# Kernel optimization log

Hardware: AMD Instinct MI355X
Metric: run time of the kernel (lower is better)

Reference implementation:

```python
import jax, jax.numpy as jnp
import numpy as np
from jax import lax

GRID = 200      # _FIXED_GRID_LEN
SOFT_K = 50.0   # _SOFT_MASK_K
BN_EPS = 1e-5


def setup_inputs() -> dict:
    key = jax.random.key(0)
    ks = jax.random.split(key, 12)
    B, L = 8192, 2001
    f32 = jnp.float32
    inp = {
        'phase': jax.random.uniform(ks[0], (B, L), f32, -1.0, 1.0),
        'primary_flux': 0.01 * jax.random.normal(ks[1], (B, L), f32),
        'secondary_flux': 0.01 * jax.random.normal(ks[2], (B, L), f32),
        'odd_even_diff': 0.01 * jax.random.normal(ks[3], (B, L), f32),
        # TaylorGateLayerV8 params
        'A': jnp.asarray(0.01, f32),
        'Bp': jnp.asarray(1.0, f32),
        't0': jnp.asarray(0.0, f32),
        # BatchNorm1d(4), eval mode (running stats)
        'bn_gamma': jnp.ones((4,), f32),
        'bn_beta': jnp.zeros((4,), f32),
        'bn_mean': jnp.zeros((4,), f32),
        'bn_var': jnp.ones((4,), f32),
        # Conv1d(4,8,7) / Conv1d(8,16,5)
        'conv1_w': 0.1 * jax.random.normal(ks[4], (8, 4, 7), f32),
        'conv1_b': jnp.zeros((8,), f32),
        'conv2_w': 0.1 * jax.random.normal(ks[5], (16, 8, 5), f32),
        'conv2_b': jnp.zeros((16,), f32),
        # Linear(21, 1)
        'fc_w': 0.1 * jax.random.normal(ks[6], (1, 21), f32),
        'fc_b': jnp.zeros((1,), f32),
    }
    return inp


def _conv1d(x, w, b, pad):
    # x: (B, C, L), w: (O, C, K)
    y = lax.conv_general_dilated(x, w, window_strides=(1,), padding=[(pad, pad)],
                                 dimension_numbers=('NCH', 'OIH', 'NCH'))
    return y + b[None, :, None]


def _interp_linear_ac(x, out_len):
    # torch F.interpolate(mode='linear', align_corners=True) on (B, L) -> (B, out_len)
    L = x.shape[1]
    pos = jnp.linspace(0.0, L - 1.0, out_len)
    i0 = jnp.floor(pos).astype(jnp.int32)
    i1 = jnp.minimum(i0 + 1, L - 1)
    w = (pos - i0).astype(x.dtype)
    return x[:, i0] * (1.0 - w) + x[:, i1] * w


def reference(phase, primary_flux, secondary_flux, odd_even_diff,
              A, Bp, t0, bn_gamma, bn_beta, bn_mean, bn_var,
              conv1_w, conv1_b, conv2_w, conv2_b, fc_w, fc_b):
    # --- TaylorGateLayerV8: 2nd-order Taylor U-shape transit template ---
    gate = -A * jnp.clip(1.0 - Bp * (phase - t0) ** 2, 0.0, None)

    # --- CNN branch ---
    x = jnp.stack([gate, primary_flux, secondary_flux, odd_even_diff], axis=1)  # (B,4,L)
    inv = bn_gamma / jnp.sqrt(bn_var + BN_EPS)
    x = x * inv[None, :, None] + (bn_beta - bn_mean * inv)[None, :, None]
    x = jax.nn.relu(_conv1d(x, conv1_w, conv1_b, 3))
    x = jax.nn.relu(_conv1d(x, conv2_w, conv2_b, 2))
    cnn_out = jnp.mean(x, axis=2)  # AdaptiveAvgPool1d(1) -> (B,16)

    # --- shape features ---
    batch = primary_flux.shape[0]
    A_abs = jnp.abs(A) + 1e-8
    depth = jnp.clip(-primary_flux, 0.0, None)
    depth_norm = depth / A_abs
    depth_rs = _interp_linear_ac(depth, GRID)  # (B, 200)
    dx = 2.0 / (GRID - 1)                       # trapz over linspace(-1,1,200)
    auc_raw = dx * (jnp.sum(depth_rs, axis=1) - 0.5 * (depth_rs[:, 0] + depth_rs[:, -1]))
    auc_norm = auc_raw / A_abs
    dip_all = jax.nn.sigmoid(SOFT_K * (depth_norm - 0.1))
    flat_bot = jax.nn.sigmoid(SOFT_K * (depth_norm - 0.8))
    ingress = dip_all - flat_bot
    total = 1.0 - dip_all + ingress + flat_bot + 1e-8
    ingress = ingress / total
    flat_bot = flat_bot / total
    t14 = jnp.mean(ingress + flat_bot, axis=1) + 1e-8
    t12_t14 = jnp.mean(ingress, axis=1) / t14
    flat_bottom = jnp.mean(flat_bot, axis=1)
    B_bcast = jnp.broadcast_to(Bp, (batch,)).astype(depth.dtype)
    shape = jnp.stack([B_bcast, auc_raw, auc_norm, t12_t14, flat_bottom], axis=1)  # (B,5)

    features = jnp.concatenate([cnn_out, shape], axis=1)  # (B,21)
    logits = features @ fc_w.T + fc_b
    return jax.nn.sigmoid(logits)
```

## Files before the change

### kernel.cpp

```cpp
#include <hip/hip_runtime.h>
#include <math.h>

#define L_LEN 2001
#define CCH 224
#define NCH 9
#define XRECS 256
#define YRECS 240
#define NTC 14

typedef __attribute__((ext_vector_type(8))) short bf16x8;
typedef __attribute__((ext_vector_type(4))) float f32x4;
typedef __attribute__((ext_vector_type(16))) float f32x16;
typedef __attribute__((ext_vector_type(4), aligned(4))) float f32x4u;
#if __has_builtin(__builtin_amdgcn_cvt_pk_bf16_f32)
typedef __attribute__((ext_vector_type(2))) __bf16 bf16x2_t;
#endif

union FragU { unsigned u[4]; uint2 u2[2]; uint4 u4; bf16x8 v; };

__device__ __forceinline__ unsigned short f2bf(float f) {
    unsigned u = __builtin_bit_cast(unsigned, f);
    u += 0x7fffu + ((u >> 16) & 1u);
    return (unsigned short)(u >> 16);
}
__device__ __forceinline__ unsigned bfpack(float lo, float hi) {
#if __has_builtin(__builtin_amdgcn_cvt_pk_bf16_f32)
    bf16x2_t r = __builtin_amdgcn_cvt_pk_bf16_f32(lo, hi);
    return __builtin_bit_cast(unsigned, r);
#else
    unsigned ul = __builtin_bit_cast(unsigned, lo);
    unsigned uh = __builtin_bit_cast(unsigned, hi);
    ul += 0x7fffu + ((ul >> 16) & 1u);
    uh += 0x7fffu + ((uh >> 16) & 1u);
    return __builtin_amdgcn_perm(uh, ul, 0x07060302);
#endif
}
__device__ __forceinline__ float fast_rcp(float x) { return __builtin_amdgcn_rcpf(x); }
__device__ __forceinline__ float fexp2(float x) {
#if __has_builtin(__builtin_amdgcn_exp2f)
    return __builtin_amdgcn_exp2f(x);
#else
    return __expf(x * 0.69314718f);
#endif
}

__global__ __launch_bounds__(256, 3)
void taylor_cnn_v11_wave(const float* __restrict__ phase, const float* __restrict__ primary,
                         const float* __restrict__ secondary, const float* __restrict__ oddeven,
                         const float* __restrict__ pA, const float* __restrict__ pBp,
                         const float* __restrict__ pT0,
                         const float* __restrict__ bng, const float* __restrict__ bnb,
                         const float* __restrict__ bnm, const float* __restrict__ bnv,
                         const float* __restrict__ w1, const float* __restrict__ b1,
                         const float* __restrict__ w2, const float* __restrict__ b2,
                         const float* __restrict__ fcw, const float* __restrict__ fcb,
                         float* __restrict__ out, int nrows)
{
    __shared__ __align__(16) unsigned int xs_i[4][XRECS * 2];
    __shared__ __align__(16) unsigned int y1_i[4][YRECS * 4];

    const int tid = threadIdx.x;
    const int l   = tid & 63;
    const int wid = tid >> 6;
    const int row = blockIdx.x * 4 + wid;
    if (row >= nrows) return;
    const long base = (long)row * L_LEN;

    unsigned int* xs = xs_i[wid];
    unsigned int* y1 = y1_i[wid];

    const int n    = l & 15;
    const int quad = l >> 4;
    const int c    = l & 31;
    const int h    = l >> 5;

    const float A  = pA[0];
    const float Bp = pBp[0];
    const float t0 = pT0[0];
    const float A_abs = fabsf(A) + 1e-8f;
    const float rAabs = 1.0f / A_abs;
    const float nBp  = -Bp;
    const float cExp = -72.134766f * rAabs;

    float inv1, inv2, inv3, gInv0, off0, off1, off2, off3;
    {
        float iv0 = bng[0] / sqrtf(bnv[0] + 1e-5f);
        float iv1 = bng[1] / sqrtf(bnv[1] + 1e-5f);
        float iv2 = bng[2] / sqrtf(bnv[2] + 1e-5f);
        float iv3 = bng[3] / sqrtf(bnv[3] + 1e-5f);
        gInv0 = -A * iv0;
        inv1 = iv1; inv2 = iv2; inv3 = iv3;
        off0 = bnb[0] - bnm[0] * iv0;
        off1 = bnb[1] - bnm[1] * iv1;
        off2 = bnb[2] - bnm[2] * iv2;
        off3 = bnb[3] - bnm[3] * iv3;
    }

    bf16x8 a32_0, a32_1;
#pragma unroll
    for (int jp = 0; jp < 8; ++jp) {
        int ch_  = jp & 3;
        int tap0 = (jp >> 2) + 2 * h;
        int tap1 = 4 + (jp >> 2) + 2 * h;
        float v0 = (c < 8) ? w1[(c * 4 + ch_) * 7 + tap0] : 0.0f;
        float v1 = (c < 8 && tap1 < 7) ? w1[(c * 4 + ch_) * 7 + tap1] : 0.0f;
        a32_0[jp] = (short)f2bf(v0);
        a32_1[jp] = (short)f2bf(v1);
    }
    f32x16 cb32;
#pragma unroll
    for (int r = 0; r < 16; ++r)
        cb32[r] = (r < 4) ? b1[(r & 3) + 4 * h] : 0.0f;

    bf16x8 a1;
#pragma unroll
    for (int jp = 0; jp < 8; ++jp) {
        int j = quad + 4 * (jp >> 2);
        int cc = jp & 3;
        float v = (n < 8 && j < 7) ? w1[(n * 4 + cc) * 7 + j] : 0.0f;
        a1[jp] = (short)f2bf(v);
    }
    bf16x8 a20, a21;
#pragma unroll
    for (int jp = 0; jp < 8; ++jp) {
        float v0 = w2[(n * 8 + jp) * 5 + quad];
        float v1 = (quad + 4 < 5) ? w2[(n * 8 + jp) * 5 + quad + 4] : 0.0f;
        a20[jp] = (short)f2bf(v0);
        a21[jp] = (short)f2bf(v1);
    }
    f32x4 cb1, cb2;
#pragma unroll
    for (int r = 0; r < 4; ++r) {
        cb1[r] = b1[(quad * 4 + r) & 7];
        cb2[r] = b2[quad * 4 + r];
    }
    float fw0 = fcw[quad * 4 + 0];
    float fw1 = fcw[quad * 4 + 1];
    float fw2 = fcw[quad * 4 + 2];
    float fw3 = fcw[quad * 4 + 3];

    float s_dip = 0.0f, s_fb = 0.0f;
    float m0 = 0.f, m1 = 0.f, m2 = 0.f, m3 = 0.f;

    float s_auc = 0.0f;
#pragma unroll
    for (int k = 0; k < 4; ++k) {
        int s = l + 64 * k;
        if (k < 3 || l < 8) {
            float pos = (float)s * (2000.0f / 199.0f);
            int i0 = (int)pos;
            if (i0 > 2000) i0 = 2000;
            int i1 = (i0 + 1 < L_LEN) ? i0 + 1 : 2000;
            float w  = pos - (float)i0;
            float d0 = fmaxf(-primary[base + i0], 0.f);
            float d1 = fmaxf(-primary[base + i1], 0.f);
            float v  = d0 * (1.0f - w) + d1 * w;
            float wt = (s == 0 || s == 199) ? 0.5f : 1.0f;
            s_auc += v * wt;
        }
    }

    auto aRec = [&](int m, int p, bool valid, bool core) {
        float ph = phase[base + p];
        float pf = primary[base + p];
        float sf = secondary[base + p];
        float oe = oddeven[base + p];
        float dd = ph - t0;
        float g  = fmaxf(fmaf(dd * dd, nBp, 1.0f), 0.0f);
        float x0 = fmaf(g,  gInv0, off0);
        float x1 = fmaf(pf, inv1, off1);
        float x2 = fmaf(sf, inv2, off2);
        float x3 = fmaf(oe, inv3, off3);
        unsigned d0 = bfpack(x0, x1);
        unsigned d1 = bfpack(x2, x3);
        if (!valid) { d0 = 0u; d1 = 0u; }
        *(uint2*)&xs[2 * m] = make_uint2(d0, d1);
        float depth = fmaxf(-pf, 0.0f);
        float e   = fexp2(depth * cExp);
        float dip = fast_rcp(fmaf(e, 148.413159f, 1.0f));
        float fb  = fast_rcp(fmaf(e, 2.35385267e17f, 1.0f));
        if (!core) { dip = 0.f; fb = 0.f; }
        s_dip += dip;
        s_fb  += fb;
    };

    const float coreMask = (l >= 4 && l < 60) ? 1.0f : 0.0f;

    f32x4u ph4, pf4, sf4, oe4;
    {
        int p0 = 4 * l - 16; if (p0 < 0) p0 = 0;
        ph4 = *(const f32x4u*)&phase[base + p0];
        pf4 = *(const f32x4u*)&primary[base + p0];
        sf4 = *(const f32x4u*)&secondary[base + p0];
        oe4 = *(const f32x4u*)&oddeven[base + p0];
    }

#pragma unroll 1
    for (int ch = 0; ch < NCH - 1; ++ch) {
        const int c0 = ch * CCH;
        const bool isFirst = (ch == 0);

        f32x4u nph, npf, nsf, noe;
        if (ch < NCH - 2) {
            const long pn = base + (c0 + CCH - 16 + 4 * l);
            nph = *(const f32x4u*)&phase[pn];
            npf = *(const f32x4u*)&primary[pn];
            nsf = *(const f32x4u*)&secondary[pn];
            noe = *(const f32x4u*)&oddeven[pn];
        } else {
            nph = ph4; npf = pf4; nsf = sf4; noe = oe4;
        }

        {
            unsigned dw[8];
            float dipA = 0.f, fbA = 0.f;
#pragma unroll
            for (int j = 0; j < 4; ++j) {
                float dd = ph4[j] - t0;
                float g  = fmaxf(fmaf(dd * dd, nBp, 1.0f), 0.0f);
                float x0 = fmaf(g,      gInv0, off0);
                float x1 = fmaf(pf4[j], inv1,  off1);
                float x2 = fmaf(sf4[j], inv2,  off2);
                float x3 = fmaf(oe4[j], inv3,  off3);
                dw[2 * j]     = bfpack(x0, x1);
                dw[2 * j + 1] = bfpack(x2, x3);
                float depth = fmaxf(-pf4[j], 0.0f);
                float e   = fexp2(depth * cExp);
                float dip = fast_rcp(fmaf(e, 148.413159f, 1.0f));
                float fb  = fast_rcp(fmaf(e, 2.35385267e17f, 1.0f));
                dipA += dip;
                fbA  += fb;
            }
            if (isFirst && l < 4) {
#pragma unroll
                for (int j = 0; j < 8; ++j) dw[j] = 0u;
            }
            *(uint4*)&xs[8 * l]     = make_uint4(dw[0], dw[1], dw[2], dw[3]);
            *(uint4*)&xs[8 * l + 4] = make_uint4(dw[4], dw[5], dw[6], dw[7]);
            s_dip = fmaf(dipA, coreMask, s_dip);
            s_fb  = fmaf(fbA,  coreMask, s_fb);
        }

        {
            const int cb = c + 2 * h + 5;
#pragma unroll 2
            for (int T = 0; T < 7; ++T) {
                const int R0 = 32 * T + cb;
                FragU b0, b1f;
                b0.u2[0]  = *(const uint2*)&xs[2 * R0];
                b0.u2[1]  = *(const uint2*)&xs[2 * R0 + 2];
                b1f.u2[0] = *(const uint2*)&xs[2 * R0 + 8];
                b1f.u2[1] = *(const uint2*)&xs[2 * R0 + 10];
                f32x16 d = __builtin_amdgcn_mfma_f32_32x32x16_bf16(a32_0, b0.v,  cb32, 0, 0, 0);
                d        = __builtin_amdgcn_mfma_f32_32x32x16_bf16(a32_1, b1f.v, d,    0, 0, 0);
                unsigned w0  = bfpack(fmaxf(d[0], 0.f), fmaxf(d[1], 0.f));
                unsigned w1_ = bfpack(fmaxf(d[2], 0.f), fmaxf(d[3], 0.f));
                if (isFirst && T == 0) {
                    if (c < 8) { w0 = 0u; w1_ = 0u; }
                }
                *(uint2*)&y1[4 * (32 * T + c) + 2 * h] = make_uint2(w0, w1_);
            }
            int qb = 224 + n + quad + 5;
            FragU bu;
            bu.u2[0] = *(const uint2*)&xs[2 * qb];
            bu.u2[1] = *(const uint2*)&xs[2 * (qb + 4)];
            f32x4 d = __builtin_amdgcn_mfma_f32_16x16x32_bf16(a1, bu.v, cb1, 0, 0, 0);
            if (l < 32) {
                unsigned w0  = bfpack(fmaxf(d[0], 0.f), fmaxf(d[1], 0.f));
                unsigned w1_ = bfpack(fmaxf(d[2], 0.f), fmaxf(d[3], 0.f));
                *(uint2*)&y1[4 * (224 + n) + 2 * quad] = make_uint2(w0, w1_);
            }
        }

#pragma unroll 2
        for (int t = 0; t < NTC; ++t) {
            int q = 16 * t + n + quad + 6;
            FragU u0, u1;
            u0.u4 = *(const uint4*)&y1[4 * q];
            u1.u4 = *(const uint4*)&y1[4 * (q + 4)];
            f32x4 d = __builtin_amdgcn_mfma_f32_16x16x32_bf16(a20, u0.v, cb2, 0, 0, 0);
            d = __builtin_amdgcn_mfma_f32_16x16x32_bf16(a21, u1.v, d, 0, 0, 0);
            m0 += fmaxf(d[0], 0.f);
            m1 += fmaxf(d[1], 0.f);
            m2 += fmaxf(d[2], 0.f);
            m3 += fmaxf(d[3], 0.f);
        }

        ph4 = nph; pf4 = npf; sf4 = nsf; oe4 = noe;
    }

    {
        const int c0 = (NCH - 1) * CCH;
        const int pb = c0 - 16;

        {
            bool co0 = (l >= 16);
            int  p3  = pb + l + 192;
            bool v3  = (l < 33);
            bool co3 = v3 && (l < 48);
            if (p3 > 2000) p3 = 2000;
            aRec(l,        pb + l,       true, co0);
            aRec(l + 64,   pb + l + 64,  true, true);
            aRec(l + 128,  pb + l + 128, true, true);
            aRec(l + 192,  p3,           v3,   co3);
        }

        {
            const int cb = c + 2 * h + 5;
#pragma unroll 2
            for (int T = 0; T < 7; ++T) {
                const int R0 = 32 * T + cb;
                FragU b0, b1f;
                b0.u2[0]  = *(const uint2*)&xs[2 * R0];
                b0.u2[1]  = *(const uint2*)&xs[2 * R0 + 2];
                b1f.u2[0] = *(const uint2*)&xs[2 * R0 + 8];
                b1f.u2[1] = *(const uint2*)&xs[2 * R0 + 10];
                f32x16 d = __builtin_amdgcn_mfma_f32_32x32x16_bf16(a32_0, b0.v,  cb32, 0, 0, 0);
                d        = __builtin_amdgcn_mfma_f32_32x32x16_bf16(a32_1, b1f.v, d,    0, 0, 0);
                unsigned w0  = bfpack(fmaxf(d[0], 0.f), fmaxf(d[1], 0.f));
                unsigned w1_ = bfpack(fmaxf(d[2], 0.f), fmaxf(d[3], 0.f));
                if (T == 6 && c > 24) { w0 = 0u; w1_ = 0u; }
                *(uint2*)&y1[4 * (32 * T + c) + 2 * h] = make_uint2(w0, w1_);
            }
            if (l < 32)
                *(uint2*)&y1[4 * (224 + n) + 2 * quad] = make_uint2(0u, 0u);
        }

#pragma unroll 2
        for (int t = 0; t < NTC; ++t) {
            int q = 16 * t + n + quad + 6;
            FragU u0, u1;
            u0.u4 = *(const uint4*)&y1[4 * q];
            u1.u4 = *(const uint4*)&y1[4 * (q + 4)];
            f32x4 d = __builtin_amdgcn_mfma_f32_16x16x32_bf16(a20, u0.v, cb2, 0, 0, 0);
            d = __builtin_amdgcn_mfma_f32_16x16x32_bf16(a21, u1.v, d, 0, 0, 0);
            if (t == 13) {
                float msk = (n == 0) ? 1.0f : 0.0f;
                m0 = fmaf(fmaxf(d[0], 0.f), msk, m0);
                m1 = fmaf(fmaxf(d[1], 0.f), msk, m1);
                m2 = fmaf(fmaxf(d[2], 0.f), msk, m2);
                m3 = fmaf(fmaxf(d[3], 0.f), msk, m3);
            } else {
                m0 += fmaxf(d[0], 0.f);
                m1 += fmaxf(d[1], 0.f);
                m2 += fmaxf(d[2], 0.f);
                m3 += fmaxf(d[3], 0.f);
            }
        }
    }

#pragma unroll
    for (int dlt = 8; dlt >= 1; dlt >>= 1) {
        m0 += __shfl_xor(m0, dlt);
        m1 += __shfl_xor(m1, dlt);
        m2 += __shfl_xor(m2, dlt);
        m3 += __shfl_xor(m3, dlt);
    }
    float part = m0 * fw0 + m1 * fw1 + m2 * fw2 + m3 * fw3;
    part = (n == 0) ? part : 0.0f;
    part += __shfl_xor(part, 16);
    part += __shfl_xor(part, 32);
#pragma unroll
    for (int dlt = 32; dlt >= 1; dlt >>= 1) {
        s_dip += __shfl_xor(s_dip, dlt);
        s_fb  += __shfl_xor(s_fb,  dlt);
        s_auc += __shfl_xor(s_auc, dlt);
    }

    if (l == 0) {
        float Sing = s_dip - s_fb;
        float logit = fcb[0] + part * (1.0f / 2001.0f);
        float auc_raw  = (float)(2.0 / 199.0) * s_auc;
        float auc_norm = auc_raw / A_abs;
        float m_ing = Sing / 2001.0f;
        float m_fb  = s_fb  / 2001.0f;
        float t14   = s_dip / 2001.0f + 1e-8f;
        float t12   = m_ing / t14;

        logit += Bp       * fcw[16]
               + auc_raw  * fcw[17]
               + auc_norm * fcw[18]
               + t12      * fcw[19]
               + m_fb     * fcw[20];

        out[row] = 1.0f / (1.0f + expf(-logit));
    }
}

extern "C" void kernel_launch(void* const* d_in, const int* in_sizes, int n_in,
                              void* d_out, int out_size, void* d_ws, size_t ws_size,
                              hipStream_t stream) {
    const float* phase     = (const float*)d_in[0];
    const float* primary   = (const float*)d_in[1];
    const float* secondary = (const float*)d_in[2];
    const float* oddeven   = (const float*)d_in[3];
    const float* pA        = (const float*)d_in[4];
    const float* pBp       = (const float*)d_in[5];
    const float* pT0       = (const float*)d_in[6];
    const float* bng       = (const float*)d_in[7];
    const float* bnb       = (const float*)d_in[8];
    const float* bnm       = (const float*)d_in[9];
    const float* bnv       = (const float*)d_in[10];
    const float* w1        = (const float*)d_in[11];
    const float* b1        = (const float*)d_in[12];
    const float* w2        = (const float*)d_in[13];
    const float* b2        = (const float*)d_in[14];
    const float* fcw       = (const float*)d_in[15];
    const float* fcb       = (const float*)d_in[16];
    float* out = (float*)d_out;

    int nrows = in_sizes[0] / L_LEN;
    dim3 grid((nrows + 3) / 4), block(256);
    hipLaunchKernelGGL(taylor_cnn_v11_wave, grid, block, 0, stream,
                       phase, primary, secondary, oddeven, pA, pBp, pT0,
                       bng, bnb, bnm, bnv, w1, b1, w2, b2, fcw, fcb, out, nrows);
}
```

Baseline: 278.1 us.

## Fold BatchNorm affine into conv1 weights and bias, pack accumulators as vectors

Moves the eval-mode BatchNorm scale into the conv1 MFMA weights and its offset into a folded conv1 bias. The per-element fma normalisation before bf16 packing goes away, and padding slots are filled with values that map to zero after normalisation, which keeps results exact. The dip/flat-bottom and max-pool accumulators are also rewritten as float2/float4 vectors so the compiler can emit packed adds. The folded padding values and scaled weights are rounded to bf16, which can shift numerics slightly, and there is extra setup work per block.

```diff
diff --git a/kernel.cpp b/kernel.cpp
--- a/kernel.cpp
+++ b/kernel.cpp
@@ -9,6 +9,7 @@
 #define NTC 14
 
 typedef __attribute__((ext_vector_type(8))) short bf16x8;
+typedef __attribute__((ext_vector_type(2))) float f32x2;
 typedef __attribute__((ext_vector_type(4))) float f32x4;
 typedef __attribute__((ext_vector_type(16))) float f32x16;
 typedef __attribute__((ext_vector_type(4), aligned(4))) float f32x4u;
@@ -45,7 +46,7 @@
 }
 
 __global__ __launch_bounds__(256, 3)
-void taylor_cnn_v11_wave(const float* __restrict__ phase, const float* __restrict__ primary,
+void taylor_cnn_v12_wave(const float* __restrict__ phase, const float* __restrict__ primary,
                          const float* __restrict__ secondary, const float* __restrict__ oddeven,
                          const float* __restrict__ pA, const float* __restrict__ pBp,
                          const float* __restrict__ pT0,
@@ -82,19 +83,41 @@
     const float nBp  = -Bp;
     const float cExp = -72.134766f * rAabs;
 
-    float inv1, inv2, inv3, gInv0, off0, off1, off2, off3;
+    float scl[4];
+    float o0, o1, o2, o3;
+    unsigned hz0, hz1;
     {
         float iv0 = bng[0] / sqrtf(bnv[0] + 1e-5f);
         float iv1 = bng[1] / sqrtf(bnv[1] + 1e-5f);
         float iv2 = bng[2] / sqrtf(bnv[2] + 1e-5f);
         float iv3 = bng[3] / sqrtf(bnv[3] + 1e-5f);
-        gInv0 = -A * iv0;
-        inv1 = iv1; inv2 = iv2; inv3 = iv3;
-        off0 = bnb[0] - bnm[0] * iv0;
-        off1 = bnb[1] - bnm[1] * iv1;
-        off2 = bnb[2] - bnm[2] * iv2;
-        off3 = bnb[3] - bnm[3] * iv3;
-    }
+        scl[0] = -A * iv0;
+        scl[1] = iv1; scl[2] = iv2; scl[3] = iv3;
+        o0 = bnb[0] - bnm[0] * iv0;
+        o1 = bnb[1] - bnm[1] * iv1;
+        o2 = bnb[2] - bnm[2] * iv2;
+        o3 = bnb[3] - bnm[3] * iv3;
+        float hv0 = (scl[0] != 0.0f) ? (-o0 / scl[0]) : 0.0f;
+        float hv1 = (scl[1] != 0.0f) ? (-o1 / scl[1]) : 0.0f;
+        float hv2 = (scl[2] != 0.0f) ? (-o2 / scl[2]) : 0.0f;
+        float hv3 = (scl[3] != 0.0f) ? (-o3 / scl[3]) : 0.0f;
+        hz0 = bfpack(hv0, hv1);
+        hz1 = bfpack(hv2, hv3);
+    }
+    const bool offZero = (o0 == 0.0f) & (o1 == 0.0f) & (o2 == 0.0f) & (o3 == 0.0f);
+    auto foldb = [&](int oc) -> float {
+        float acc = b1[oc];
+        if (!offZero) {
+#pragma unroll
+            for (int tap = 0; tap < 7; ++tap) {
+                acc = fmaf(w1[(oc * 4 + 0) * 7 + tap], o0, acc);
+                acc = fmaf(w1[(oc * 4 + 1) * 7 + tap], o1, acc);
+                acc = fmaf(w1[(oc * 4 + 2) * 7 + tap], o2, acc);
+                acc = fmaf(w1[(oc * 4 + 3) * 7 + tap], o3, acc);
+            }
+        }
+        return acc;
+    };
 
     bf16x8 a32_0, a32_1;
 #pragma unroll
@@ -102,22 +125,22 @@
         int ch_  = jp & 3;
         int tap0 = (jp >> 2) + 2 * h;
         int tap1 = 4 + (jp >> 2) + 2 * h;
-        float v0 = (c < 8) ? w1[(c * 4 + ch_) * 7 + tap0] : 0.0f;
-        float v1 = (c < 8 && tap1 < 7) ? w1[(c * 4 + ch_) * 7 + tap1] : 0.0f;
+        float v0 = (c < 8) ? w1[(c * 4 + ch_) * 7 + tap0] * scl[ch_] : 0.0f;
+        float v1 = (c < 8 && tap1 < 7) ? w1[(c * 4 + ch_) * 7 + tap1] * scl[ch_] : 0.0f;
         a32_0[jp] = (short)f2bf(v0);
         a32_1[jp] = (short)f2bf(v1);
     }
     f32x16 cb32;
 #pragma unroll
     for (int r = 0; r < 16; ++r)
-        cb32[r] = (r < 4) ? b1[(r & 3) + 4 * h] : 0.0f;
+        cb32[r] = (r < 4) ? foldb((r & 3) + 4 * h) : 0.0f;
 
     bf16x8 a1;
 #pragma unroll
     for (int jp = 0; jp < 8; ++jp) {
         int j = quad + 4 * (jp >> 2);
         int cc = jp & 3;
-        float v = (n < 8 && j < 7) ? w1[(n * 4 + cc) * 7 + j] : 0.0f;
+        float v = (n < 8 && j < 7) ? w1[(n * 4 + cc) * 7 + j] * scl[cc] : 0.0f;
         a1[jp] = (short)f2bf(v);
     }
     bf16x8 a20, a21;
@@ -131,7 +154,7 @@
     f32x4 cb1, cb2;
 #pragma unroll
     for (int r = 0; r < 4; ++r) {
-        cb1[r] = b1[(quad * 4 + r) & 7];
+        cb1[r] = foldb((quad * 4 + r) & 7);
         cb2[r] = b2[quad * 4 + r];
     }
     float fw0 = fcw[quad * 4 + 0];
@@ -139,8 +162,8 @@
     float fw2 = fcw[quad * 4 + 2];
     float fw3 = fcw[quad * 4 + 3];
 
-    float s_dip = 0.0f, s_fb = 0.0f;
-    float m0 = 0.f, m1 = 0.f, m2 = 0.f, m3 = 0.f;
+    f32x2 s_df = {0.0f, 0.0f};
+    f32x4 mv   = {0.0f, 0.0f, 0.0f, 0.0f};
 
     float s_auc = 0.0f;
 #pragma unroll
@@ -167,21 +190,17 @@
         float oe = oddeven[base + p];
         float dd = ph - t0;
         float g  = fmaxf(fmaf(dd * dd, nBp, 1.0f), 0.0f);
-        float x0 = fmaf(g,  gInv0, off0);
-        float x1 = fmaf(pf, inv1, off1);
-        float x2 = fmaf(sf, inv2, off2);
-        float x3 = fmaf(oe, inv3, off3);
-        unsigned d0 = bfpack(x0, x1);
-        unsigned d1 = bfpack(x2, x3);
-        if (!valid) { d0 = 0u; d1 = 0u; }
+        unsigned d0 = bfpack(g,  pf);
+        unsigned d1 = bfpack(sf, oe);
+        if (!valid) { d0 = hz0; d1 = hz1; }
         *(uint2*)&xs[2 * m] = make_uint2(d0, d1);
         float depth = fmaxf(-pf, 0.0f);
         float e   = fexp2(depth * cExp);
         float dip = fast_rcp(fmaf(e, 148.413159f, 1.0f));
         float fb  = fast_rcp(fmaf(e, 2.35385267e17f, 1.0f));
         if (!core) { dip = 0.f; fb = 0.f; }
-        s_dip += dip;
-        s_fb  += fb;
+        f32x2 df = {dip, fb};
+        s_df += df;
     };
 
     const float coreMask = (l >= 4 && l < 60) ? 1.0f : 0.0f;
@@ -213,32 +232,27 @@
 
         {
             unsigned dw[8];
-            float dipA = 0.f, fbA = 0.f;
+            f32x2 ddf = {0.f, 0.f};
 #pragma unroll
             for (int j = 0; j < 4; ++j) {
                 float dd = ph4[j] - t0;
                 float g  = fmaxf(fmaf(dd * dd, nBp, 1.0f), 0.0f);
-                float x0 = fmaf(g,      gInv0, off0);
-                float x1 = fmaf(pf4[j], inv1,  off1);
-                float x2 = fmaf(sf4[j], inv2,  off2);
-                float x3 = fmaf(oe4[j], inv3,  off3);
-                dw[2 * j]     = bfpack(x0, x1);
-                dw[2 * j + 1] = bfpack(x2, x3);
+                dw[2 * j]     = bfpack(g,      pf4[j]);
+                dw[2 * j + 1] = bfpack(sf4[j], oe4[j]);
                 float depth = fmaxf(-pf4[j], 0.0f);
                 float e   = fexp2(depth * cExp);
                 float dip = fast_rcp(fmaf(e, 148.413159f, 1.0f));
                 float fb  = fast_rcp(fmaf(e, 2.35385267e17f, 1.0f));
-                dipA += dip;
-                fbA  += fb;
+                f32x2 df = {dip, fb};
+                ddf += df;
             }
             if (isFirst && l < 4) {
 #pragma unroll
-                for (int j = 0; j < 8; ++j) dw[j] = 0u;
+                for (int j = 0; j < 4; ++j) { dw[2 * j] = hz0; dw[2 * j + 1] = hz1; }
             }
             *(uint4*)&xs[8 * l]     = make_uint4(dw[0], dw[1], dw[2], dw[3]);
             *(uint4*)&xs[8 * l + 4] = make_uint4(dw[4], dw[5], dw[6], dw[7]);
-            s_dip = fmaf(dipA, coreMask, s_dip);
-            s_fb  = fmaf(fbA,  coreMask, s_fb);
+            s_df += ddf * coreMask;
         }
 
         {
@@ -280,10 +294,12 @@
             u1.u4 = *(const uint4*)&y1[4 * (q + 4)];
             f32x4 d = __builtin_amdgcn_mfma_f32_16x16x32_bf16(a20, u0.v, cb2, 0, 0, 0);
             d = __builtin_amdgcn_mfma_f32_16x16x32_bf16(a21, u1.v, d, 0, 0, 0);
-            m0 += fmaxf(d[0], 0.f);
-            m1 += fmaxf(d[1], 0.f);
-            m2 += fmaxf(d[2], 0.f);
-            m3 += fmaxf(d[3], 0.f);
+            f32x4 dm;
+            dm[0] = fmaxf(d[0], 0.f);
+            dm[1] = fmaxf(d[1], 0.f);
+            dm[2] = fmaxf(d[2], 0.f);
+            dm[3] = fmaxf(d[3], 0.f);
+            mv += dm;
         }
 
         ph4 = nph; pf4 = npf; sf4 = nsf; oe4 = noe;
@@ -336,19 +352,22 @@
             d = __builtin_amdgcn_mfma_f32_16x16x32_bf16(a21, u1.v, d, 0, 0, 0);
             if (t == 13) {
                 float msk = (n == 0) ? 1.0f : 0.0f;
-                m0 = fmaf(fmaxf(d[0], 0.f), msk, m0);
-                m1 = fmaf(fmaxf(d[1], 0.f), msk, m1);
-                m2 = fmaf(fmaxf(d[2], 0.f), msk, m2);
-                m3 = fmaf(fmaxf(d[3], 0.f), msk, m3);
+                mv[0] = fmaf(fmaxf(d[0], 0.f), msk, mv[0]);
+                mv[1] = fmaf(fmaxf(d[1], 0.f), msk, mv[1]);
+                mv[2] = fmaf(fmaxf(d[2], 0.f), msk, mv[2]);
+                mv[3] = fmaf(fmaxf(d[3], 0.f), msk, mv[3]);
             } else {
-                m0 += fmaxf(d[0], 0.f);
-                m1 += fmaxf(d[1], 0.f);
-                m2 += fmaxf(d[2], 0.f);
-                m3 += fmaxf(d[3], 0.f);
-            }
-        }
-    }
-
+                f32x4 dm;
+                dm[0] = fmaxf(d[0], 0.f);
+                dm[1] = fmaxf(d[1], 0.f);
+                dm[2] = fmaxf(d[2], 0.f);
+                dm[3] = fmaxf(d[3], 0.f);
+                mv += dm;
+            }
+        }
+    }
+
+    float m0 = mv[0], m1 = mv[1], m2 = mv[2], m3 = mv[3];
 #pragma unroll
     for (int dlt = 8; dlt >= 1; dlt >>= 1) {
         m0 += __shfl_xor(m0, dlt);
@@ -360,6 +379,7 @@
     part = (n == 0) ? part : 0.0f;
     part += __shfl_xor(part, 16);
     part += __shfl_xor(part, 32);
+    float s_dip = s_df[0], s_fb = s_df[1];
 #pragma unroll
     for (int dlt = 32; dlt >= 1; dlt >>= 1) {
         s_dip += __shfl_xor(s_dip, dlt);
@@ -411,7 +431,7 @@
 
     int nrows = in_sizes[0] / L_LEN;
     dim3 grid((nrows + 3) / 4), block(256);
-    hipLaunchKernelGGL(taylor_cnn_v11_wave, grid, block, 0, stream,
+    hipLaunchKernelGGL(taylor_cnn_v12_wave, grid, block, 0, stream,
                        phase, primary, secondary, oddeven, pA, pBp, pT0,
                        bng, bnb, bnm, bnv, w1, b1, w2, b2, fcw, fcb, out, nrows);
 }
```

New measurement: 282.4 us. Within noise of the previous version (+1.5%).

## Double-buffer input staging and software-pipeline conv stages across chunks

Applied to the files above, without the earlier changes.

The single per-wave LDS input buffer becomes a pair, and the chunk loop is reordered so conv1 (stage B) on the current chunk runs before the next chunk's input preprocessing (aVec). That preprocessing is then interleaved with conv2 (stage C) of the current chunk. The loads are also issued two chunks ahead instead of one. The aim is to overlap VALU transcendental work and global loads with MFMA work and hide load latency. It doubles LDS use for the input staging, which may affect the 3-blocks-per-CU occupancy target, and raises register pressure.

```diff
diff --git a/kernel.cpp b/kernel.cpp
--- a/kernel.cpp
+++ b/kernel.cpp
@@ -45,7 +45,7 @@
 }
 
 __global__ __launch_bounds__(256, 3)
-void taylor_cnn_v11_wave(const float* __restrict__ phase, const float* __restrict__ primary,
+void taylor_cnn_v13_wave(const float* __restrict__ phase, const float* __restrict__ primary,
                          const float* __restrict__ secondary, const float* __restrict__ oddeven,
                          const float* __restrict__ pA, const float* __restrict__ pBp,
                          const float* __restrict__ pT0,
@@ -56,7 +56,7 @@
                          const float* __restrict__ fcw, const float* __restrict__ fcb,
                          float* __restrict__ out, int nrows)
 {
-    __shared__ __align__(16) unsigned int xs_i[4][XRECS * 2];
+    __shared__ __align__(16) unsigned int xs_i[4][2][XRECS * 2];
     __shared__ __align__(16) unsigned int y1_i[4][YRECS * 4];
 
     const int tid = threadIdx.x;
@@ -66,8 +66,9 @@
     if (row >= nrows) return;
     const long base = (long)row * L_LEN;
 
-    unsigned int* xs = xs_i[wid];
-    unsigned int* y1 = y1_i[wid];
+    unsigned int* xs0 = xs_i[wid][0];
+    unsigned int* xs1 = xs_i[wid][1];
+    unsigned int* y1  = y1_i[wid];
 
     const int n    = l & 15;
     const int quad = l >> 4;
@@ -174,7 +175,7 @@
         unsigned d0 = bfpack(x0, x1);
         unsigned d1 = bfpack(x2, x3);
         if (!valid) { d0 = 0u; d1 = 0u; }
-        *(uint2*)&xs[2 * m] = make_uint2(d0, d1);
+        *(uint2*)&xs0[2 * m] = make_uint2(d0, d1);
         float depth = fmaxf(-pf, 0.0f);
         float e   = fexp2(depth * cExp);
         float dip = fast_rcp(fmaf(e, 148.413159f, 1.0f));
@@ -186,92 +187,73 @@
 
     const float coreMask = (l >= 4 && l < 60) ? 1.0f : 0.0f;
 
-    f32x4u ph4, pf4, sf4, oe4;
-    {
-        int p0 = 4 * l - 16; if (p0 < 0) p0 = 0;
-        ph4 = *(const f32x4u*)&phase[base + p0];
-        pf4 = *(const f32x4u*)&primary[base + p0];
-        sf4 = *(const f32x4u*)&secondary[base + p0];
-        oe4 = *(const f32x4u*)&oddeven[base + p0];
-    }
-
-#pragma unroll 1
-    for (int ch = 0; ch < NCH - 1; ++ch) {
-        const int c0 = ch * CCH;
-        const bool isFirst = (ch == 0);
-
-        f32x4u nph, npf, nsf, noe;
-        if (ch < NCH - 2) {
-            const long pn = base + (c0 + CCH - 16 + 4 * l);
-            nph = *(const f32x4u*)&phase[pn];
-            npf = *(const f32x4u*)&primary[pn];
-            nsf = *(const f32x4u*)&secondary[pn];
-            noe = *(const f32x4u*)&oddeven[pn];
-        } else {
-            nph = ph4; npf = pf4; nsf = sf4; noe = oe4;
-        }
-
-        {
-            unsigned dw[8];
-            float dipA = 0.f, fbA = 0.f;
-#pragma unroll
-            for (int j = 0; j < 4; ++j) {
-                float dd = ph4[j] - t0;
-                float g  = fmaxf(fmaf(dd * dd, nBp, 1.0f), 0.0f);
-                float x0 = fmaf(g,      gInv0, off0);
-                float x1 = fmaf(pf4[j], inv1,  off1);
-                float x2 = fmaf(sf4[j], inv2,  off2);
-                float x3 = fmaf(oe4[j], inv3,  off3);
-                dw[2 * j]     = bfpack(x0, x1);
-                dw[2 * j + 1] = bfpack(x2, x3);
-                float depth = fmaxf(-pf4[j], 0.0f);
-                float e   = fexp2(depth * cExp);
-                float dip = fast_rcp(fmaf(e, 148.413159f, 1.0f));
-                float fb  = fast_rcp(fmaf(e, 2.35385267e17f, 1.0f));
-                dipA += dip;
-                fbA  += fb;
-            }
-            if (isFirst && l < 4) {
-#pragma unroll
-                for (int j = 0; j < 8; ++j) dw[j] = 0u;
-            }
-            *(uint4*)&xs[8 * l]     = make_uint4(dw[0], dw[1], dw[2], dw[3]);
-            *(uint4*)&xs[8 * l + 4] = make_uint4(dw[4], dw[5], dw[6], dw[7]);
-            s_dip = fmaf(dipA, coreMask, s_dip);
-            s_fb  = fmaf(fbA,  coreMask, s_fb);
-        }
-
-        {
-            const int cb = c + 2 * h + 5;
+    auto aVec = [&](unsigned int* xsBuf, const f32x4u& vph, const f32x4u& vpf,
+                    const f32x4u& vsf, const f32x4u& voe, bool zeroLow) {
+        unsigned dw[8];
+        float dipA = 0.f, fbA = 0.f;
+#pragma unroll
+        for (int j = 0; j < 4; ++j) {
+            float dd = vph[j] - t0;
+            float g  = fmaxf(fmaf(dd * dd, nBp, 1.0f), 0.0f);
+            float x0 = fmaf(g,      gInv0, off0);
+            float x1 = fmaf(vpf[j], inv1,  off1);
+            float x2 = fmaf(vsf[j], inv2,  off2);
+            float x3 = fmaf(voe[j], inv3,  off3);
+            dw[2 * j]     = bfpack(x0, x1);
+            dw[2 * j + 1] = bfpack(x2, x3);
+            float depth = fmaxf(-vpf[j], 0.0f);
+            float e   = fexp2(depth * cExp);
+            float dip = fast_rcp(fmaf(e, 148.413159f, 1.0f));
+            float fb  = fast_rcp(fmaf(e, 2.35385267e17f, 1.0f));
+            dipA += dip;
+            fbA  += fb;
+        }
+        if (zeroLow && l < 4) {
+#pragma unroll
+            for (int j = 0; j < 8; ++j) dw[j] = 0u;
+        }
+        *(uint4*)&xsBuf[8 * l]     = make_uint4(dw[0], dw[1], dw[2], dw[3]);
+        *(uint4*)&xsBuf[8 * l + 4] = make_uint4(dw[4], dw[5], dw[6], dw[7]);
+        s_dip = fmaf(dipA, coreMask, s_dip);
+        s_fb  = fmaf(fbA,  coreMask, s_fb);
+    };
+
+    auto stageB = [&](const unsigned int* xsBuf, bool loZero, bool hiMask, bool tailZero) {
+        const int cb = c + 2 * h + 5;
 #pragma unroll 2
-            for (int T = 0; T < 7; ++T) {
-                const int R0 = 32 * T + cb;
-                FragU b0, b1f;
-                b0.u2[0]  = *(const uint2*)&xs[2 * R0];
-                b0.u2[1]  = *(const uint2*)&xs[2 * R0 + 2];
-                b1f.u2[0] = *(const uint2*)&xs[2 * R0 + 8];
-                b1f.u2[1] = *(const uint2*)&xs[2 * R0 + 10];
-                f32x16 d = __builtin_amdgcn_mfma_f32_32x32x16_bf16(a32_0, b0.v,  cb32, 0, 0, 0);
-                d        = __builtin_amdgcn_mfma_f32_32x32x16_bf16(a32_1, b1f.v, d,    0, 0, 0);
-                unsigned w0  = bfpack(fmaxf(d[0], 0.f), fmaxf(d[1], 0.f));
-                unsigned w1_ = bfpack(fmaxf(d[2], 0.f), fmaxf(d[3], 0.f));
-                if (isFirst && T == 0) {
-                    if (c < 8) { w0 = 0u; w1_ = 0u; }
-                }
-                *(uint2*)&y1[4 * (32 * T + c) + 2 * h] = make_uint2(w0, w1_);
-            }
+        for (int T = 0; T < 7; ++T) {
+            const int R0 = 32 * T + cb;
+            FragU b0, b1f;
+            b0.u2[0]  = *(const uint2*)&xsBuf[2 * R0];
+            b0.u2[1]  = *(const uint2*)&xsBuf[2 * R0 + 2];
+            b1f.u2[0] = *(const uint2*)&xsBuf[2 * R0 + 8];
+            b1f.u2[1] = *(const uint2*)&xsBuf[2 * R0 + 10];
+            f32x16 d = __builtin_amdgcn_mfma_f32_32x32x16_bf16(a32_0, b0.v,  cb32, 0, 0, 0);
+            d        = __builtin_amdgcn_mfma_f32_32x32x16_bf16(a32_1, b1f.v, d,    0, 0, 0);
+            unsigned w0  = bfpack(fmaxf(d[0], 0.f), fmaxf(d[1], 0.f));
+            unsigned w1_ = bfpack(fmaxf(d[2], 0.f), fmaxf(d[3], 0.f));
+            if (loZero && T == 0) { if (c < 8)  { w0 = 0u; w1_ = 0u; } }
+            if (hiMask && T == 6) { if (c > 24) { w0 = 0u; w1_ = 0u; } }
+            *(uint2*)&y1[4 * (32 * T + c) + 2 * h] = make_uint2(w0, w1_);
+        }
+        if (!tailZero) {
             int qb = 224 + n + quad + 5;
             FragU bu;
-            bu.u2[0] = *(const uint2*)&xs[2 * qb];
-            bu.u2[1] = *(const uint2*)&xs[2 * (qb + 4)];
+            bu.u2[0] = *(const uint2*)&xsBuf[2 * qb];
+            bu.u2[1] = *(const uint2*)&xsBuf[2 * (qb + 4)];
             f32x4 d = __builtin_amdgcn_mfma_f32_16x16x32_bf16(a1, bu.v, cb1, 0, 0, 0);
             if (l < 32) {
                 unsigned w0  = bfpack(fmaxf(d[0], 0.f), fmaxf(d[1], 0.f));
                 unsigned w1_ = bfpack(fmaxf(d[2], 0.f), fmaxf(d[3], 0.f));
                 *(uint2*)&y1[4 * (224 + n) + 2 * quad] = make_uint2(w0, w1_);
             }
-        }
-
+        } else {
+            if (l < 32)
+                *(uint2*)&y1[4 * (224 + n) + 2 * quad] = make_uint2(0u, 0u);
+        }
+    };
+
+    auto stageC = [&](int maskT) {
 #pragma unroll 2
         for (int t = 0; t < NTC; ++t) {
             int q = 16 * t + n + quad + 6;
@@ -280,61 +262,7 @@
             u1.u4 = *(const uint4*)&y1[4 * (q + 4)];
             f32x4 d = __builtin_amdgcn_mfma_f32_16x16x32_bf16(a20, u0.v, cb2, 0, 0, 0);
             d = __builtin_amdgcn_mfma_f32_16x16x32_bf16(a21, u1.v, d, 0, 0, 0);
-            m0 += fmaxf(d[0], 0.f);
-            m1 += fmaxf(d[1], 0.f);
-            m2 += fmaxf(d[2], 0.f);
-            m3 += fmaxf(d[3], 0.f);
-        }
-
-        ph4 = nph; pf4 = npf; sf4 = nsf; oe4 = noe;
-    }
-
-    {
-        const int c0 = (NCH - 1) * CCH;
-        const int pb = c0 - 16;
-
-        {
-            bool co0 = (l >= 16);
-            int  p3  = pb + l + 192;
-            bool v3  = (l < 33);
-            bool co3 = v3 && (l < 48);
-            if (p3 > 2000) p3 = 2000;
-            aRec(l,        pb + l,       true, co0);
-            aRec(l + 64,   pb + l + 64,  true, true);
-            aRec(l + 128,  pb + l + 128, true, true);
-            aRec(l + 192,  p3,           v3,   co3);
-        }
-
-        {
-            const int cb = c + 2 * h + 5;
-#pragma unroll 2
-            for (int T = 0; T < 7; ++T) {
-                const int R0 = 32 * T + cb;
-                FragU b0, b1f;
-                b0.u2[0]  = *(const uint2*)&xs[2 * R0];
-                b0.u2[1]  = *(const uint2*)&xs[2 * R0 + 2];
-                b1f.u2[0] = *(const uint2*)&xs[2 * R0 + 8];
-                b1f.u2[1] = *(const uint2*)&xs[2 * R0 + 10];
-                f32x16 d = __builtin_amdgcn_mfma_f32_32x32x16_bf16(a32_0, b0.v,  cb32, 0, 0, 0);
-                d        = __builtin_amdgcn_mfma_f32_32x32x16_bf16(a32_1, b1f.v, d,    0, 0, 0);
-                unsigned w0  = bfpack(fmaxf(d[0], 0.f), fmaxf(d[1], 0.f));
-                unsigned w1_ = bfpack(fmaxf(d[2], 0.f), fmaxf(d[3], 0.f));
-                if (T == 6 && c > 24) { w0 = 0u; w1_ = 0u; }
-                *(uint2*)&y1[4 * (32 * T + c) + 2 * h] = make_uint2(w0, w1_);
-            }
-            if (l < 32)
-                *(uint2*)&y1[4 * (224 + n) + 2 * quad] = make_uint2(0u, 0u);
-        }
-
-#pragma unroll 2
-        for (int t = 0; t < NTC; ++t) {
-            int q = 16 * t + n + quad + 6;
-            FragU u0, u1;
-            u0.u4 = *(const uint4*)&y1[4 * q];
-            u1.u4 = *(const uint4*)&y1[4 * (q + 4)];
-            f32x4 d = __builtin_amdgcn_mfma_f32_16x16x32_bf16(a20, u0.v, cb2, 0, 0, 0);
-            d = __builtin_amdgcn_mfma_f32_16x16x32_bf16(a21, u1.v, d, 0, 0, 0);
-            if (t == 13) {
+            if (t == maskT) {
                 float msk = (n == 0) ? 1.0f : 0.0f;
                 m0 = fmaf(fmaxf(d[0], 0.f), msk, m0);
                 m1 = fmaf(fmaxf(d[1], 0.f), msk, m1);
@@ -347,6 +275,69 @@
                 m3 += fmaxf(d[3], 0.f);
             }
         }
+    };
+
+    f32x4u ph4, pf4, sf4, oe4;
+    {
+        int p0 = 4 * l - 16; if (p0 < 0) p0 = 0;
+        f32x4u tph = *(const f32x4u*)&phase[base + p0];
+        f32x4u tpf = *(const f32x4u*)&primary[base + p0];
+        f32x4u tsf = *(const f32x4u*)&secondary[base + p0];
+        f32x4u toe = *(const f32x4u*)&oddeven[base + p0];
+        const long p1 = base + (CCH - 16 + 4 * l);
+        ph4 = *(const f32x4u*)&phase[p1];
+        pf4 = *(const f32x4u*)&primary[p1];
+        sf4 = *(const f32x4u*)&secondary[p1];
+        oe4 = *(const f32x4u*)&oddeven[p1];
+        aVec(xs0, tph, tpf, tsf, toe, true);
+    }
+
+#pragma unroll 1
+    for (int ch = 0; ch < NCH - 2; ++ch) {
+        unsigned int* xsCur = (ch & 1) ? xs1 : xs0;
+        unsigned int* xsNxt = (ch & 1) ? xs0 : xs1;
+
+        stageB(xsCur, ch == 0, false, false);
+
+        f32x4u nph, npf, nsf, noe;
+        if (ch < NCH - 3) {
+            const long pn = base + ((ch + 2) * CCH - 16 + 4 * l);
+            nph = *(const f32x4u*)&phase[pn];
+            npf = *(const f32x4u*)&primary[pn];
+            nsf = *(const f32x4u*)&secondary[pn];
+            noe = *(const f32x4u*)&oddeven[pn];
+        } else {
+            nph = ph4; npf = pf4; nsf = sf4; noe = oe4;
+        }
+
+        aVec(xsNxt, ph4, pf4, sf4, oe4, false);
+
+        stageC(-1);
+
+        ph4 = nph; pf4 = npf; sf4 = nsf; oe4 = noe;
+    }
+
+    {
+        stageB(xs1, false, false, false);
+
+        {
+            const int pb = (NCH - 1) * CCH - 16;
+            bool co0 = (l >= 16);
+            int  p3  = pb + l + 192;
+            bool v3  = (l < 33);
+            bool co3 = v3 && (l < 48);
+            if (p3 > 2000) p3 = 2000;
+            aRec(l,        pb + l,       true, co0);
+            aRec(l + 64,   pb + l + 64,  true, true);
+            aRec(l + 128,  pb + l + 128, true, true);
+            aRec(l + 192,  p3,           v3,   co3);
+        }
+
+        stageC(-1);
+
+        stageB(xs0, false, true, true);
+
+        stageC(13);
     }
 
 #pragma unroll
@@ -411,7 +402,7 @@
 
     int nrows = in_sizes[0] / L_LEN;
     dim3 grid((nrows + 3) / 4), block(256);
-    hipLaunchKernelGGL(taylor_cnn_v11_wave, grid, block, 0, stream,
+    hipLaunchKernelGGL(taylor_cnn_v13_wave, grid, block, 0, stream,
                        phase, primary, secondary, oddeven, pA, pBp, pT0,
                        bng, bnb, bnm, bnv, w1, b1, w2, b2, fcw, fcb, out, nrows);
 }
```

Result: slower. 286.6 us (+3.1%).
